# Kernel tuning notes

Hardware: AMD Instinct MI355X
Metric: run time of the kernel (lower is better)

## Reference

```python
import jax, jax.numpy as jnp
import numpy as np

VOCAB = 10000
EMBED = 512
HIDDEN = 1024
FEAT = 2048
PAD_IDX = 0


def setup_inputs() -> dict:
    key = jax.random.key(0)
    ks = jax.random.split(key, 12)
    s = lambda fan_in: 1.0 / np.sqrt(fan_in)
    features = jax.random.normal(ks[0], (64, FEAT), dtype=jnp.float32)
    captions = jax.random.randint(ks[1], (64, 32), 0, VOCAB)
    embed_table = jax.random.normal(ks[2], (VOCAB, EMBED), dtype=jnp.float32) * 0.02
    embed_table = embed_table.at[PAD_IDX].set(0.0)  # padding_idx row is zero
    W_init_h = jax.random.uniform(ks[3], (HIDDEN, FEAT), jnp.float32, -s(FEAT), s(FEAT))
    b_init_h = jnp.zeros((HIDDEN,), jnp.float32)
    W_init_c = jax.random.uniform(ks[4], (HIDDEN, FEAT), jnp.float32, -s(FEAT), s(FEAT))
    b_init_c = jnp.zeros((HIDDEN,), jnp.float32)
    W_ih = jax.random.uniform(ks[5], (4 * HIDDEN, EMBED), jnp.float32, -s(HIDDEN), s(HIDDEN))
    b_ih = jax.random.uniform(ks[6], (4 * HIDDEN,), jnp.float32, -s(HIDDEN), s(HIDDEN))
    W_hh = jax.random.uniform(ks[7], (4 * HIDDEN, HIDDEN), jnp.float32, -s(HIDDEN), s(HIDDEN))
    b_hh = jax.random.uniform(ks[8], (4 * HIDDEN,), jnp.float32, -s(HIDDEN), s(HIDDEN))
    W_fc = jax.random.uniform(ks[9], (VOCAB, HIDDEN), jnp.float32, -s(HIDDEN), s(HIDDEN))
    b_fc = jax.random.uniform(ks[10], (VOCAB,), jnp.float32, -s(HIDDEN), s(HIDDEN))
    return {
        "features": features, "captions": captions, "embed_table": embed_table,
        "W_init_h": W_init_h, "b_init_h": b_init_h, "W_init_c": W_init_c, "b_init_c": b_init_c,
        "W_ih": W_ih, "b_ih": b_ih, "W_hh": W_hh, "b_hh": b_hh,
        "W_fc": W_fc, "b_fc": b_fc,
    }


def _lstm_cell(x, h, c, W_ih, b_ih, W_hh, b_hh):
    # torch LSTMCell gate order: i, f, g, o
    gates = x @ W_ih.T + b_ih + h @ W_hh.T + b_hh  # [B, 4H]
    i, f, g, o = jnp.split(gates, 4, axis=-1)
    i = jax.nn.sigmoid(i)
    f = jax.nn.sigmoid(f)
    g = jnp.tanh(g)
    o = jax.nn.sigmoid(o)
    c = f * c + i * g
    h = o * jnp.tanh(c)
    return h, c


def reference(features, captions, embed_table, W_init_h, b_init_h, W_init_c, b_init_c,
              W_ih, b_ih, W_hh, b_hh, W_fc, b_fc):
    h0 = features @ W_init_h.T + b_init_h  # [B, H]
    c0 = features @ W_init_c.T + b_init_c  # [B, H]
    emb = embed_table[captions]            # [B, T, E]
    emb_t = jnp.swapaxes(emb, 0, 1)        # [T, B, E] for scan over time

    def step(carry, x_t):
        h, c = carry
        h, c = _lstm_cell(x_t, h, c, W_ih, b_ih, W_hh, b_hh)
        out = jax.nn.sigmoid(h @ W_fc.T + b_fc)  # [B, V]
        return (h, c), out

    _, outs = jax.lax.scan(step, (h0, c0), emb_t)
    return outs  # [T, B, V] matching torch.stack(dim=0)
```

## Files before the change

kernel.cpp:

```cpp
#include <hip/hip_runtime.h>


#define B_  64
#define T_  32
#define E_  512
#define H_  1024
#define V_  10000
#define F_  2048

typedef short short8 __attribute__((ext_vector_type(8)));
typedef float floatx4 __attribute__((ext_vector_type(4)));

__device__ __forceinline__ float bf2f(unsigned short u) {
  union { unsigned int i; float f; } c; c.i = ((unsigned int)u) << 16; return c.f;
}
__device__ __forceinline__ unsigned short f2bf(float f) {
  union { float f; unsigned int i; } c; c.f = f;
  unsigned int x = c.i;
  return (unsigned short)((x + 0x7fffu + ((x >> 16) & 1u)) >> 16);
}
__device__ __forceinline__ float sigmoidf_(float x) {
  return 1.0f / (1.0f + __expf(-x));
}
__device__ __forceinline__ void gl_lds16(const unsigned short* g, unsigned short* l) {
  __builtin_amdgcn_global_load_lds(
      (const __attribute__((address_space(1))) unsigned int*)g,
      (__attribute__((address_space(3))) unsigned int*)l, 16, 0, 0);
}
__device__ __forceinline__ int xcd_swz(int lin, int nwg) {
  if (nwg < 8) return lin;
  int q = nwg >> 3, r = nwg & 7;
  int xcd = lin & 7, pos = lin >> 3;
  return (xcd < r ? xcd * (q + 1) : r * (q + 1) + (xcd - r) * q) + pos;
}

#define C_WIH  524288
#define C_WHH  1048576
#define C_WFC  2560000
#define C_WI0  524288
#define C_WC0  524288
#define C_FEA  32768
#define C_TOT  (C_WIH + C_WHH + C_WFC + C_WI0 + C_WC0 + C_FEA)

__global__ __launch_bounds__(256) void cvt_all(
    const float* __restrict__ s0, const float* __restrict__ s1,
    const float* __restrict__ s2, const float* __restrict__ s3,
    const float* __restrict__ s4, const float* __restrict__ s5,
    unsigned short* __restrict__ d0, unsigned short* __restrict__ d1,
    unsigned short* __restrict__ d2, unsigned short* __restrict__ d3,
    unsigned short* __restrict__ d4, unsigned short* __restrict__ d5) {
  int i = blockIdx.x * blockDim.x + threadIdx.x;
  int stride = gridDim.x * blockDim.x;
  for (; i < C_TOT; i += stride) {
    const float* s; unsigned short* d; int j = i;
    if (j < C_WIH)            { s = s0; d = d0; }
    else if ((j -= C_WIH) < C_WHH) { s = s1; d = d1; }
    else if ((j -= C_WHH) < C_WFC) { s = s2; d = d2; }
    else if ((j -= C_WFC) < C_WI0) { s = s3; d = d3; }
    else if ((j -= C_WI0) < C_WC0) { s = s4; d = d4; }
    else { j -= C_WC0; s = s5; d = d5; }
    float4 v = ((const float4*)s)[j];
    ushort4 o;
    o.x = f2bf(v.x); o.y = f2bf(v.y); o.z = f2bf(v.z); o.w = f2bf(v.w);
    ((ushort4*)d)[j] = o;
  }
}

__global__ __launch_bounds__(128) void embed_gather(
    const float* __restrict__ table, const int* __restrict__ captions,
    unsigned short* __restrict__ out) {
  int row = blockIdx.x;
  int t = row >> 6, b = row & 63;
  int idx = captions[b * T_ + t];
  const float4* src = (const float4*)(table + (size_t)idx * E_);
  ushort4* dst = (ushort4*)(out + (size_t)row * E_);
  for (int e = threadIdx.x; e < E_ / 4; e += blockDim.x) {
    float4 v = src[e];
    ushort4 o;
    o.x = f2bf(v.x); o.y = f2bf(v.y); o.z = f2bf(v.z); o.w = f2bf(v.w);
    dst[e] = o;
  }
}

template <int ACT_SIGMOID, int OUT_BF16, int OUT_INIT>
__global__ __launch_bounds__(256) void mfma_gemm128(
    const unsigned short* __restrict__ A, const unsigned short* __restrict__ W,
    const float* __restrict__ bias1, const float* __restrict__ bias2,
    void* __restrict__ out, void* __restrict__ out2, int M, int N, int K) {
  __shared__ unsigned short At[2][128 * 32];
  __shared__ unsigned short Wt[2][128 * 32];

  const int tid  = threadIdx.x;
  const int lane = tid & 63;
  const int wave = tid >> 6;
  const int l15  = lane & 15;
  const int quad = lane >> 4;
  const int wm   = (wave >> 1) * 64;
  const int wn   = (wave & 1) * 64;

  const int gx  = gridDim.x;
  const int nwg = gx * gridDim.y;
  const int wg  = xcd_swz(blockIdx.y * gx + blockIdx.x, nwg);
  const int m0  = (wg % gx) * 128;
  const int n0  = (wg / gx) * 128;
  const int ksl = (quad ^ (l15 & 3)) * 8;

  const int c0i = tid, c1i = tid + 256;
  const int ar0 = c0i >> 2, ak0 = (((c0i & 3) ^ (ar0 & 3)) * 8);
  const int ar1 = c1i >> 2, ak1 = (((c1i & 3) ^ (ar1 & 3)) * 8);
  int am0 = m0 + ar0; if (am0 > M - 1) am0 = M - 1;
  int am1 = m0 + ar1; if (am1 > M - 1) am1 = M - 1;
  int wn0 = n0 + ar0; if (wn0 > N - 1) wn0 = N - 1;
  int wn1 = n0 + ar1; if (wn1 > N - 1) wn1 = N - 1;
  const unsigned short* Ag0 = A + (size_t)am0 * K + ak0;
  const unsigned short* Ag1 = A + (size_t)am1 * K + ak1;
  const unsigned short* Wg0 = W + (size_t)wn0 * K + ak0;
  const unsigned short* Wg1 = W + (size_t)wn1 * K + ak1;

  floatx4 acc[4][4];
#pragma unroll
  for (int i = 0; i < 4; ++i)
#pragma unroll
    for (int j = 0; j < 4; ++j) acc[i][j] = (floatx4){0.f, 0.f, 0.f, 0.f};

  gl_lds16(Ag0, &At[0][c0i * 8]);
  gl_lds16(Ag1, &At[0][c1i * 8]);
  gl_lds16(Wg0, &Wt[0][c0i * 8]);
  gl_lds16(Wg1, &Wt[0][c1i * 8]);
  __syncthreads();

  int cur = 0;
  for (int k0 = 0; k0 < K; k0 += 32) {
    const int kn = k0 + 32;
    if (kn < K) {
      const int nb = cur ^ 1;
      gl_lds16(Ag0 + kn, &At[nb][c0i * 8]);
      gl_lds16(Ag1 + kn, &At[nb][c1i * 8]);
      gl_lds16(Wg0 + kn, &Wt[nb][c0i * 8]);
      gl_lds16(Wg1 + kn, &Wt[nb][c1i * 8]);
    }
    short8 a[4], b[4];
#pragma unroll
    for (int mt = 0; mt < 4; ++mt)
      a[mt] = *(const short8*)&At[cur][(wm + mt * 16 + l15) * 32 + ksl];
#pragma unroll
    for (int nt = 0; nt < 4; ++nt)
      b[nt] = *(const short8*)&Wt[cur][(wn + nt * 16 + l15) * 32 + ksl];
#pragma unroll
    for (int mt = 0; mt < 4; ++mt)
#pragma unroll
      for (int nt = 0; nt < 4; ++nt)
        acc[mt][nt] = __builtin_amdgcn_mfma_f32_16x16x32_bf16(a[mt], b[nt], acc[mt][nt], 0, 0, 0);
    __syncthreads();
    cur ^= 1;
  }

#pragma unroll
  for (int nt = 0; nt < 4; ++nt) {
    int col = n0 + wn + nt * 16 + l15;
    if (col >= N) continue;
    float bsum;
    if (OUT_INIT)
      bsum = (col < H_) ? bias1[col] : bias2[col - H_];
    else
      bsum = (bias1 ? bias1[col] : 0.f) + (bias2 ? bias2[col] : 0.f);
#pragma unroll
    for (int mt = 0; mt < 4; ++mt) {
#pragma unroll
      for (int r = 0; r < 4; ++r) {
        int m = m0 + wm + mt * 16 + quad * 4 + r;
        if (m >= M) continue;
        float v = acc[mt][nt][r] + bsum;
        if (ACT_SIGMOID) v = sigmoidf_(v);
        if (OUT_INIT) {
          if (col < H_)
            ((unsigned short*)out)[(size_t)m * H_ + col] = f2bf(v);
          else
            ((float*)out2)[(size_t)m * H_ + (col - H_)] = v;
        } else if (OUT_BF16) {
          ((unsigned short*)out)[(size_t)m * N + col] = f2bf(v);
        } else {
          ((float*)out)[(size_t)m * N + col] = v;
        }
      }
    }
  }
}

#define WSPAD2 1032
__global__ __launch_bounds__(512, 2) void lstm_step(
    const unsigned short* __restrict__ W_hh_b,
    const unsigned short* __restrict__ gx_t,
    float* __restrict__ c,
    const unsigned short* __restrict__ h_in,
    unsigned short* __restrict__ h_out) {
  __shared__ unsigned short Ws[32 * WSPAD2];
  __shared__ float gbuf[4][32][33];

  const int tid  = threadIdx.x;
  const int lane = tid & 63;
  const int wave = tid >> 6;
  const int l15  = lane & 15;
  const int quad = lane >> 4;
  const int kb   = quad * 8;
  const int cg   = blockIdx.x >> 1;
  const int bh   = blockIdx.x & 1;
  const int colbase = cg * 8;
  const int kq   = wave >> 1;
  const int mt   = wave & 1;

#pragma unroll
  for (int it = 0; it < 8; ++it) {
    int u = wave * 8 + it;
    int n = u >> 1, half = u & 1;
    int grow = (n >> 3) * H_ + colbase + (n & 7);
    gl_lds16(W_hh_b + (size_t)grow * H_ + half * 512 + lane * 8,
             &Ws[n * WSPAD2 + half * 512]);
  }

  const unsigned short* hp =
      h_in + (size_t)(bh * 32 + mt * 16 + l15) * H_ + kq * 256 + kb;
  short8 hx[8];
#pragma unroll
  for (int i = 0; i < 8; ++i)
    hx[i] = *(const short8*)(hp + i * 32);

  const int bq = tid >> 3, cj = tid & 7;
  float gxi = 0.f, gxf = 0.f, gxg = 0.f, gxo = 0.f, c_old = 0.f;
  if (tid < 256) {
    const int gb = bh * 32 + bq;
    const unsigned short* gxp = gx_t + (size_t)gb * (4 * H_) + colbase + cj;
    gxi = bf2f(gxp[0 * H_]);
    gxf = bf2f(gxp[1 * H_]);
    gxg = bf2f(gxp[2 * H_]);
    gxo = bf2f(gxp[3 * H_]);
    c_old = c[gb * H_ + colbase + cj];
  }

  __syncthreads();

  const unsigned short* wb0 = &Ws[(size_t)(l15)      * WSPAD2 + kq * 256 + kb];
  const unsigned short* wb1 = &Ws[(size_t)(16 + l15) * WSPAD2 + kq * 256 + kb];
  floatx4 A0 = (floatx4){0.f, 0.f, 0.f, 0.f}, A1 = A0;
#pragma unroll
  for (int i = 0; i < 8; ++i) {
    short8 w0 = *(const short8*)(wb0 + i * 32);
    short8 w1 = *(const short8*)(wb1 + i * 32);
    A0 = __builtin_amdgcn_mfma_f32_16x16x32_bf16(hx[i], w0, A0, 0, 0, 0);
    A1 = __builtin_amdgcn_mfma_f32_16x16x32_bf16(hx[i], w1, A1, 0, 0, 0);
  }

#pragma unroll
  for (int r = 0; r < 4; ++r) {
    gbuf[kq][mt * 16 + quad * 4 + r][l15]      = A0[r];
    gbuf[kq][mt * 16 + quad * 4 + r][16 + l15] = A1[r];
  }
  __syncthreads();

  if (tid < 256) {
    const int gb = bh * 32 + bq;
    float gi = gbuf[0][bq][ 0 + cj] + gbuf[1][bq][ 0 + cj]
             + gbuf[2][bq][ 0 + cj] + gbuf[3][bq][ 0 + cj] + gxi;
    float gf = gbuf[0][bq][ 8 + cj] + gbuf[1][bq][ 8 + cj]
             + gbuf[2][bq][ 8 + cj] + gbuf[3][bq][ 8 + cj] + gxf;
    float gg = gbuf[0][bq][16 + cj] + gbuf[1][bq][16 + cj]
             + gbuf[2][bq][16 + cj] + gbuf[3][bq][16 + cj] + gxg;
    float go = gbuf[0][bq][24 + cj] + gbuf[1][bq][24 + cj]
             + gbuf[2][bq][24 + cj] + gbuf[3][bq][24 + cj] + gxo;
    gi = sigmoidf_(gi);
    gf = sigmoidf_(gf);
    gg = tanhf(gg);
    go = sigmoidf_(go);
    int ci = gb * H_ + colbase + cj;
    float cn = gf * c_old + gi * gg;
    c[ci] = cn;
    h_out[ci] = f2bf(go * tanhf(cn));
  }
}

extern "C" void kernel_launch(void* const* d_in, const int* in_sizes, int n_in,
                              void* d_out, int out_size, void* d_ws, size_t ws_size,
                              hipStream_t stream) {
  const float* features    = (const float*)d_in[0];
  const int*   captions    = (const int*)d_in[1];
  const float* embed_table = (const float*)d_in[2];
  const float* W_init_h    = (const float*)d_in[3];
  const float* b_init_h    = (const float*)d_in[4];
  const float* W_init_c    = (const float*)d_in[5];
  const float* b_init_c    = (const float*)d_in[6];
  const float* W_ih        = (const float*)d_in[7];
  const float* b_ih        = (const float*)d_in[8];
  const float* W_hh        = (const float*)d_in[9];
  const float* b_hh        = (const float*)d_in[10];
  const float* W_fc        = (const float*)d_in[11];
  const float* b_fc        = (const float*)d_in[12];
  float* out = (float*)d_out;

  char* ws = (char*)d_ws;
  auto alloc = [&](size_t bytes) -> char* {
    char* p = ws;
    ws += (bytes + 255) & ~(size_t)255;
    return p;
  };
  unsigned short* W_ih_b  = (unsigned short*)alloc((size_t)4 * H_ * E_ * 2);
  unsigned short* W_hh_b  = (unsigned short*)alloc((size_t)4 * H_ * H_ * 2);
  unsigned short* W_fc_b  = (unsigned short*)alloc((size_t)V_ * H_ * 2);
  unsigned short* Wih0_b  = (unsigned short*)alloc((size_t)H_ * F_ * 2);
  unsigned short* Wic0_b  = (unsigned short*)alloc((size_t)H_ * F_ * 2);
  unsigned short* feat_b  = (unsigned short*)alloc((size_t)B_ * F_ * 2);
  unsigned short* emb_b   = (unsigned short*)alloc((size_t)T_ * B_ * E_ * 2);
  unsigned short* gx_b    = (unsigned short*)alloc((size_t)T_ * B_ * 4 * H_ * 2);
  unsigned short* h_all   = (unsigned short*)alloc((size_t)(T_ + 1) * B_ * H_ * 2);
  float*          c_f32   = (float*)alloc((size_t)B_ * H_ * 4);
  (void)ws_size; (void)in_sizes; (void)n_in; (void)out_size; (void)Wic0_b;

  hipLaunchKernelGGL(cvt_all, dim3(4096), dim3(256), 0, stream,
                     W_ih, W_hh, W_fc, W_init_h, W_init_c, features,
                     W_ih_b, W_hh_b, W_fc_b, Wih0_b, Wic0_b, feat_b);

  hipLaunchKernelGGL(embed_gather, dim3(T_ * B_), dim3(128), 0, stream,
                     embed_table, captions, emb_b);

  hipLaunchKernelGGL((mfma_gemm128<0, 1, 1>), dim3(1, 2 * H_ / 128), dim3(256), 0, stream,
                     feat_b, Wih0_b, b_init_h, b_init_c,
                     (void*)h_all, (void*)c_f32, B_, 2 * H_, F_);

  hipLaunchKernelGGL((mfma_gemm128<0, 1, 0>), dim3(T_ * B_ / 128, 4 * H_ / 128), dim3(256), 0, stream,
                     emb_b, W_ih_b, b_ih, b_hh, (void*)gx_b, (void*)nullptr,
                     T_ * B_, 4 * H_, E_);

  for (int t = 0; t < T_; ++t) {
    hipLaunchKernelGGL(lstm_step, dim3(2 * H_ / 8), dim3(512), 0, stream,
                       W_hh_b,
                       gx_b + (size_t)t * B_ * 4 * H_,
                       c_f32,
                       h_all + (size_t)t * B_ * H_,
                       h_all + (size_t)(t + 1) * B_ * H_);
  }

  hipLaunchKernelGGL((mfma_gemm128<1, 0, 0>), dim3(T_ * B_ / 128, (V_ + 127) / 128), dim3(256), 0, stream,
                     h_all + (size_t)B_ * H_, W_fc_b, b_fc, (const float*)nullptr,
                     (void*)out, (void*)nullptr, T_ * B_, V_, H_);
}
```

Before: 503.3 us.

## Fuse per-timestep LSTM launches into one persistent cooperative kernel with grid barrier

```diff
diff --git a/kernel.cpp b/kernel.cpp
--- a/kernel.cpp
+++ b/kernel.cpp
@@ -48,7 +48,10 @@
     const float* __restrict__ s4, const float* __restrict__ s5,
     unsigned short* __restrict__ d0, unsigned short* __restrict__ d1,
     unsigned short* __restrict__ d2, unsigned short* __restrict__ d3,
-    unsigned short* __restrict__ d4, unsigned short* __restrict__ d5) {
+    unsigned short* __restrict__ d4, unsigned short* __restrict__ d5,
+    unsigned int* __restrict__ bar) {
+  if (blockIdx.x == 0 && threadIdx.x == 0)
+    __hip_atomic_store(bar, 0u, __ATOMIC_RELAXED, __HIP_MEMORY_SCOPE_AGENT);
   int i = blockIdx.x * blockDim.x + threadIdx.x;
   int stride = gridDim.x * blockDim.x;
   for (; i < C_TOT; i += stride) {
@@ -188,12 +191,12 @@
 }
 
 #define WSPAD2 1032
-__global__ __launch_bounds__(512, 2) void lstm_step(
+__global__ __launch_bounds__(512, 2) void lstm_persistent(
     const unsigned short* __restrict__ W_hh_b,
-    const unsigned short* __restrict__ gx_t,
-    float* __restrict__ c,
-    const unsigned short* __restrict__ h_in,
-    unsigned short* __restrict__ h_out) {
+    const unsigned short* __restrict__ gx_b,
+    const float* __restrict__ c0_f32,
+    unsigned short* __restrict__ h_all,
+    unsigned int* __restrict__ bar) {
   __shared__ unsigned short Ws[32 * WSPAD2];
   __shared__ float gbuf[4][32][33];
 
@@ -218,63 +221,100 @@
              &Ws[n * WSPAD2 + half * 512]);
   }
 
-  const unsigned short* hp =
-      h_in + (size_t)(bh * 32 + mt * 16 + l15) * H_ + kq * 256 + kb;
-  short8 hx[8];
-#pragma unroll
-  for (int i = 0; i < 8; ++i)
-    hx[i] = *(const short8*)(hp + i * 32);
-
-  const int bq = tid >> 3, cj = tid & 7;
-  float gxi = 0.f, gxf = 0.f, gxg = 0.f, gxo = 0.f, c_old = 0.f;
-  if (tid < 256) {
-    const int gb = bh * 32 + bq;
-    const unsigned short* gxp = gx_t + (size_t)gb * (4 * H_) + colbase + cj;
-    gxi = bf2f(gxp[0 * H_]);
-    gxf = bf2f(gxp[1 * H_]);
-    gxg = bf2f(gxp[2 * H_]);
-    gxo = bf2f(gxp[3 * H_]);
-    c_old = c[gb * H_ + colbase + cj];
-  }
-
-  __syncthreads();
-
+  const int bq = tid >> 2;
+  const int cp = tid & 3;
+  const int gb = bh * 32 + bq;
+  float cA = 0.f, cB = 0.f;
+  if (tid < 128) {
+    float2 cv = *(const float2*)(c0_f32 + (size_t)gb * H_ + colbase + 2 * cp);
+    cA = cv.x; cB = cv.y;
+  }
+
+  const unsigned short* hbase =
+      h_all + (size_t)(bh * 32 + mt * 16 + l15) * H_ + kq * 256 + kb;
   const unsigned short* wb0 = &Ws[(size_t)(l15)      * WSPAD2 + kq * 256 + kb];
   const unsigned short* wb1 = &Ws[(size_t)(16 + l15) * WSPAD2 + kq * 256 + kb];
-  floatx4 A0 = (floatx4){0.f, 0.f, 0.f, 0.f}, A1 = A0;
-#pragma unroll
-  for (int i = 0; i < 8; ++i) {
-    short8 w0 = *(const short8*)(wb0 + i * 32);
-    short8 w1 = *(const short8*)(wb1 + i * 32);
-    A0 = __builtin_amdgcn_mfma_f32_16x16x32_bf16(hx[i], w0, A0, 0, 0, 0);
-    A1 = __builtin_amdgcn_mfma_f32_16x16x32_bf16(hx[i], w1, A1, 0, 0, 0);
-  }
-
-#pragma unroll
-  for (int r = 0; r < 4; ++r) {
-    gbuf[kq][mt * 16 + quad * 4 + r][l15]      = A0[r];
-    gbuf[kq][mt * 16 + quad * 4 + r][16 + l15] = A1[r];
-  }
+
   __syncthreads();
 
-  if (tid < 256) {
-    const int gb = bh * 32 + bq;
-    float gi = gbuf[0][bq][ 0 + cj] + gbuf[1][bq][ 0 + cj]
-             + gbuf[2][bq][ 0 + cj] + gbuf[3][bq][ 0 + cj] + gxi;
-    float gf = gbuf[0][bq][ 8 + cj] + gbuf[1][bq][ 8 + cj]
-             + gbuf[2][bq][ 8 + cj] + gbuf[3][bq][ 8 + cj] + gxf;
-    float gg = gbuf[0][bq][16 + cj] + gbuf[1][bq][16 + cj]
-             + gbuf[2][bq][16 + cj] + gbuf[3][bq][16 + cj] + gxg;
-    float go = gbuf[0][bq][24 + cj] + gbuf[1][bq][24 + cj]
-             + gbuf[2][bq][24 + cj] + gbuf[3][bq][24 + cj] + gxo;
-    gi = sigmoidf_(gi);
-    gf = sigmoidf_(gf);
-    gg = tanhf(gg);
-    go = sigmoidf_(go);
-    int ci = gb * H_ + colbase + cj;
-    float cn = gf * c_old + gi * gg;
-    c[ci] = cn;
-    h_out[ci] = f2bf(go * tanhf(cn));
+  for (int t = 0; t < T_; ++t) {
+    const unsigned short* hp = hbase + (size_t)t * (B_ * H_);
+    short8 hx[8];
+#pragma unroll
+    for (int i = 0; i < 8; ++i)
+      asm volatile("global_load_dwordx4 %0, %1, off sc0 sc1"
+                   : "=v"(hx[i]) : "v"(hp + i * 32) : "memory");
+
+    unsigned int ui = 0, uf = 0, ug = 0, uo = 0;
+    if (tid < 128) {
+      const unsigned short* gxp =
+          gx_b + (size_t)t * (B_ * 4 * H_) + (size_t)gb * (4 * H_) + colbase + 2 * cp;
+      ui = *(const unsigned int*)(gxp + 0 * H_);
+      uf = *(const unsigned int*)(gxp + 1 * H_);
+      ug = *(const unsigned int*)(gxp + 2 * H_);
+      uo = *(const unsigned int*)(gxp + 3 * H_);
+    }
+
+    asm volatile("s_waitcnt vmcnt(0)" ::: "memory");
+    __builtin_amdgcn_sched_barrier(0);
+
+    floatx4 A0 = (floatx4){0.f, 0.f, 0.f, 0.f}, A1 = A0;
+#pragma unroll
+    for (int i = 0; i < 8; ++i) {
+      short8 w0 = *(const short8*)(wb0 + i * 32);
+      short8 w1 = *(const short8*)(wb1 + i * 32);
+      A0 = __builtin_amdgcn_mfma_f32_16x16x32_bf16(hx[i], w0, A0, 0, 0, 0);
+      A1 = __builtin_amdgcn_mfma_f32_16x16x32_bf16(hx[i], w1, A1, 0, 0, 0);
+    }
+#pragma unroll
+    for (int r = 0; r < 4; ++r) {
+      gbuf[kq][mt * 16 + quad * 4 + r][l15]      = A0[r];
+      gbuf[kq][mt * 16 + quad * 4 + r][16 + l15] = A1[r];
+    }
+    __syncthreads();
+
+    if (tid < 128) {
+      const int c0c = 2 * cp, c1c = 2 * cp + 1;
+      float giA = gbuf[0][bq][ 0 + c0c] + gbuf[1][bq][ 0 + c0c]
+                + gbuf[2][bq][ 0 + c0c] + gbuf[3][bq][ 0 + c0c] + bf2f((unsigned short)(ui & 0xffff));
+      float gfA = gbuf[0][bq][ 8 + c0c] + gbuf[1][bq][ 8 + c0c]
+                + gbuf[2][bq][ 8 + c0c] + gbuf[3][bq][ 8 + c0c] + bf2f((unsigned short)(uf & 0xffff));
+      float ggA = gbuf[0][bq][16 + c0c] + gbuf[1][bq][16 + c0c]
+                + gbuf[2][bq][16 + c0c] + gbuf[3][bq][16 + c0c] + bf2f((unsigned short)(ug & 0xffff));
+      float goA = gbuf[0][bq][24 + c0c] + gbuf[1][bq][24 + c0c]
+                + gbuf[2][bq][24 + c0c] + gbuf[3][bq][24 + c0c] + bf2f((unsigned short)(uo & 0xffff));
+      float giB = gbuf[0][bq][ 0 + c1c] + gbuf[1][bq][ 0 + c1c]
+                + gbuf[2][bq][ 0 + c1c] + gbuf[3][bq][ 0 + c1c] + bf2f((unsigned short)(ui >> 16));
+      float gfB = gbuf[0][bq][ 8 + c1c] + gbuf[1][bq][ 8 + c1c]
+                + gbuf[2][bq][ 8 + c1c] + gbuf[3][bq][ 8 + c1c] + bf2f((unsigned short)(uf >> 16));
+      float ggB = gbuf[0][bq][16 + c1c] + gbuf[1][bq][16 + c1c]
+                + gbuf[2][bq][16 + c1c] + gbuf[3][bq][16 + c1c] + bf2f((unsigned short)(ug >> 16));
+      float goB = gbuf[0][bq][24 + c1c] + gbuf[1][bq][24 + c1c]
+                + gbuf[2][bq][24 + c1c] + gbuf[3][bq][24 + c1c] + bf2f((unsigned short)(uo >> 16));
+      giA = sigmoidf_(giA); gfA = sigmoidf_(gfA); ggA = tanhf(ggA); goA = sigmoidf_(goA);
+      giB = sigmoidf_(giB); gfB = sigmoidf_(gfB); ggB = tanhf(ggB); goB = sigmoidf_(goB);
+      cA = gfA * cA + giA * ggA;
+      cB = gfB * cB + giB * ggB;
+      float hA = goA * tanhf(cA);
+      float hB = goB * tanhf(cB);
+      unsigned int hv = (unsigned int)f2bf(hA) | ((unsigned int)f2bf(hB) << 16);
+      unsigned int* hop = (unsigned int*)(h_all + (size_t)(t + 1) * (B_ * H_)
+                                          + (size_t)gb * H_ + colbase + 2 * cp);
+      asm volatile("global_store_dword %0, %1, off sc0 sc1"
+                   :: "v"(hop), "v"(hv) : "memory");
+      asm volatile("s_waitcnt vmcnt(0)" ::: "memory");
+    }
+    __syncthreads();
+
+    if (t < T_ - 1) {
+      if (tid == 0) {
+        atomicAdd(bar, 1u);
+        const unsigned int tgt = 256u * (unsigned int)(t + 1);
+        while (__hip_atomic_load(bar, __ATOMIC_RELAXED, __HIP_MEMORY_SCOPE_AGENT) < tgt)
+          __builtin_amdgcn_s_sleep(1);
+      }
+      __syncthreads();
+    }
   }
 }
 
@@ -312,11 +352,12 @@
   unsigned short* gx_b    = (unsigned short*)alloc((size_t)T_ * B_ * 4 * H_ * 2);
   unsigned short* h_all   = (unsigned short*)alloc((size_t)(T_ + 1) * B_ * H_ * 2);
   float*          c_f32   = (float*)alloc((size_t)B_ * H_ * 4);
+  unsigned int*   bar     = (unsigned int*)alloc(256);
   (void)ws_size; (void)in_sizes; (void)n_in; (void)out_size; (void)Wic0_b;
 
   hipLaunchKernelGGL(cvt_all, dim3(4096), dim3(256), 0, stream,
                      W_ih, W_hh, W_fc, W_init_h, W_init_c, features,
-                     W_ih_b, W_hh_b, W_fc_b, Wih0_b, Wic0_b, feat_b);
+                     W_ih_b, W_hh_b, W_fc_b, Wih0_b, Wic0_b, feat_b, bar);
 
   hipLaunchKernelGGL(embed_gather, dim3(T_ * B_), dim3(128), 0, stream,
                      embed_table, captions, emb_b);
@@ -329,13 +370,11 @@
                      emb_b, W_ih_b, b_ih, b_hh, (void*)gx_b, (void*)nullptr,
                      T_ * B_, 4 * H_, E_);
 
-  for (int t = 0; t < T_; ++t) {
-    hipLaunchKernelGGL(lstm_step, dim3(2 * H_ / 8), dim3(512), 0, stream,
-                       W_hh_b,
-                       gx_b + (size_t)t * B_ * 4 * H_,
-                       c_f32,
-                       h_all + (size_t)t * B_ * H_,
-                       h_all + (size_t)(t + 1) * B_ * H_);
+  {
+    void* args[] = {(void*)&W_hh_b, (void*)&gx_b, (void*)&c_f32,
+                    (void*)&h_all, (void*)&bar};
+    hipLaunchCooperativeKernel((const void*)lstm_persistent,
+                               dim3(2 * H_ / 8), dim3(512), args, 0, stream);
   }
 
   hipLaunchKernelGGL((mfma_gemm128<1, 0, 0>), dim3(T_ * B_ / 128, (V_ + 127) / 128), dim3(256), 0, stream,
```

Result: slower. 641.5 us (+27.5%).
